# Performance work log

Measured on AMD Instinct MI355X. Metric: run time of the kernel, lower is better.

## Reference

```python
import jax, jax.numpy as jnp
import numpy as np


def setup_inputs() -> dict:
    key = jax.random.key(0)
    k1, k2 = jax.random.split(key)
    C, K, H, W = 512, 150, 512, 512
    feats_chw = jax.random.normal(k1, (C, H, W), dtype=jnp.float32)
    class_logits_chw = jax.random.normal(k2, (K, H, W), dtype=jnp.float32)
    return {"feats_chw": feats_chw, "class_logits_chw": class_logits_chw}


def reference(feats_chw, class_logits_chw):
    Cf, H, W = feats_chw.shape
    K = class_logits_chw.shape[0]
    N = H * W
    feats = feats_chw.reshape(Cf, N).T                      # (N, C)
    logits = class_logits_chw.reshape(K, N).T               # (N, K)
    probs = jax.nn.softmax(logits, axis=-1)                 # softmax over classes per pixel
    # normalize each class column over all N pixels
    weights = probs / jnp.clip(jnp.sum(probs, axis=0, keepdims=True), 1e-06)
    context = jnp.einsum('nk,nc->kc', weights, feats)        # (K, C)
    return context
```

## Files before the change

kernel.cpp:

```cpp
#include <hip/hip_runtime.h>
#include <hip/hip_bf16.h>


#define N_PIX (512 * 512)
#define K_CLS 150
#define C_DIM 512
#define NBLK 256
#define PIX_PER_BLK (N_PIX / NBLK)
#define CHUNK 64
#define NCHUNK (PIX_PER_BLK / CHUNK)

typedef short short8 __attribute__((ext_vector_type(8)));
typedef float floatx4 __attribute__((ext_vector_type(4)));

__device__ __forceinline__ unsigned short f2bf(float x) {
  unsigned u = __builtin_bit_cast(unsigned, x);
  u += 0x7FFFu + ((u >> 16) & 1u);
  return (unsigned short)(u >> 16);
}

__device__ __forceinline__ void async_ld4(const float* g, float* l) {
  __builtin_amdgcn_global_load_lds(
      (const __attribute__((address_space(1))) void*)g,
      (__attribute__((address_space(3))) void*)l, 4, 0, 0);
}

__global__ __launch_bounds__(512) void sg_main(
    const float* __restrict__ feats, const float* __restrict__ logits,
    float* __restrict__ ctx, float* __restrict__ colsum_g)
{
  __shared__ float lraw[2][K_CLS][CHUNK];
  __shared__ unsigned short atile[20 * 64 * 8];
  __shared__ float part[8][64];
  __shared__ float colsum_lds[K_CLS];

  const int tid  = threadIdx.x;
  const int w    = tid >> 6;
  const int lane = tid & 63;
  const int quad = lane >> 4;
  const int l15  = lane & 15;
  const int nbase = blockIdx.x * PIX_PER_BLK;

  for (int i = tid; i < 20 * 64 * 8 / 2; i += 512) ((unsigned*)atile)[i] = 0u;
  if (tid < K_CLS) colsum_lds[tid] = 0.f;

  floatx4 acc[4][10];
#pragma unroll
  for (int j = 0; j < 4; ++j)
#pragma unroll
    for (int rg = 0; rg < 10; ++rg)
      acc[j][rg] = (floatx4){0.f, 0.f, 0.f, 0.f};

#pragma unroll
  for (int i = 0; i < 19; ++i) {
    const int k = w + 8 * i;
    if (k < K_CLS)
      async_ld4(logits + (size_t)k * N_PIX + nbase + lane, &lraw[0][k][0]);
  }

  for (int ci = 0; ci < NCHUNK; ++ci) {
    __syncthreads();
    const int buf = ci & 1;
    const int n0  = nbase + ci * CHUNK;

    floatx4 breg[8];
#pragma unroll
    for (int j = 0; j < 4; ++j) {
      const float* bp = feats + (size_t)((w + 8 * j) * 16 + l15) * N_PIX + n0 + quad * 8;
      breg[2 * j]     = *(const floatx4*)bp;
      breg[2 * j + 1] = *(const floatx4*)(bp + 4);
    }

    float s_part = 0.f;
#pragma unroll
    for (int i = 0; i < 19; ++i) {
      const int k = w + 8 * i;
      if (k < K_CLS) s_part += __expf(lraw[buf][k][lane]);
    }
    part[w][lane] = s_part;
    __syncthreads();
    float s = 0.f;
#pragma unroll
    for (int ww = 0; ww < 8; ++ww) s += part[ww][lane];
    const float rs = 1.0f / s;

#pragma unroll
    for (int i = 0; i < 19; ++i) {
      const int k = w + 8 * i;
      if (k < K_CLS) {
        const float p = __expf(lraw[buf][k][lane]) * rs;
        const int fid = ((k >> 4) << 1) + (lane >> 5);
        const int lin = (k & 15) | (((lane >> 3) & 3) << 4);
        atile[(fid * 64 + lin) * 8 + (lane & 7)] = f2bf(p);
        float r = p;
        r += __shfl_xor(r, 32);
        r += __shfl_xor(r, 16);
        r += __shfl_xor(r, 8);
        r += __shfl_xor(r, 4);
        r += __shfl_xor(r, 2);
        r += __shfl_xor(r, 1);
        if (lane == 0) colsum_lds[k] += r;
      }
    }
    __syncthreads();

    short8 bfrag[4];
#pragma unroll
    for (int j = 0; j < 4; ++j) {
      floatx4 lo = breg[2 * j], hi = breg[2 * j + 1];
      short8 f;
      f[0] = f2bf(lo[0]); f[1] = f2bf(lo[1]); f[2] = f2bf(lo[2]); f[3] = f2bf(lo[3]);
      f[4] = f2bf(hi[0]); f[5] = f2bf(hi[1]); f[6] = f2bf(hi[2]); f[7] = f2bf(hi[3]);
      bfrag[j] = f;
    }

#pragma unroll
    for (int j = 0; j < 4; ++j) {
      const float* bp = feats + (size_t)((w + 8 * j) * 16 + l15) * N_PIX + n0 + 32 + quad * 8;
      breg[2 * j]     = *(const floatx4*)bp;
      breg[2 * j + 1] = *(const floatx4*)(bp + 4);
    }

    if (ci + 1 < NCHUNK) {
#pragma unroll
      for (int i = 0; i < 19; ++i) {
        const int k = w + 8 * i;
        if (k < K_CLS)
          async_ld4(logits + (size_t)k * N_PIX + n0 + CHUNK + lane, &lraw[buf ^ 1][k][0]);
      }
    }

#pragma unroll
    for (int rg = 0; rg < 10; ++rg) {
      short8 afrag = *(const short8*)&atile[((rg * 2 + 0) * 64 + lane) * 8];
#pragma unroll
      for (int j = 0; j < 4; ++j)
        acc[j][rg] = __builtin_amdgcn_mfma_f32_16x16x32_bf16(afrag, bfrag[j], acc[j][rg], 0, 0, 0);
    }

#pragma unroll
    for (int j = 0; j < 4; ++j) {
      floatx4 lo = breg[2 * j], hi = breg[2 * j + 1];
      short8 f;
      f[0] = f2bf(lo[0]); f[1] = f2bf(lo[1]); f[2] = f2bf(lo[2]); f[3] = f2bf(lo[3]);
      f[4] = f2bf(hi[0]); f[5] = f2bf(hi[1]); f[6] = f2bf(hi[2]); f[7] = f2bf(hi[3]);
      bfrag[j] = f;
    }

#pragma unroll
    for (int rg = 0; rg < 10; ++rg) {
      short8 afrag = *(const short8*)&atile[((rg * 2 + 1) * 64 + lane) * 8];
#pragma unroll
      for (int j = 0; j < 4; ++j)
        acc[j][rg] = __builtin_amdgcn_mfma_f32_16x16x32_bf16(afrag, bfrag[j], acc[j][rg], 0, 0, 0);
    }
  }

#pragma unroll
  for (int j = 0; j < 4; ++j) {
    const int c = ((w + 8 * j) << 4) + l15;
#pragma unroll
    for (int rg = 0; rg < 10; ++rg) {
#pragma unroll
      for (int r = 0; r < 4; ++r) {
        const int row = rg * 16 + quad * 4 + r;
        if (row < K_CLS) atomicAdd(&ctx[row * C_DIM + c], acc[j][rg][r]);
      }
    }
  }
  __syncthreads();
  if (tid < K_CLS) atomicAdd(&colsum_g[tid], colsum_lds[tid]);
}

__global__ void sg_epi(const float* __restrict__ ctx, const float* __restrict__ colsum,
                       float* __restrict__ out)
{
  const int idx = blockIdx.x * 256 + threadIdx.x;
  if (idx < K_CLS * C_DIM) {
    const float d = fmaxf(colsum[idx >> 9], 1e-6f);
    out[idx] = ctx[idx] / d;
  }
}

extern "C" void kernel_launch(void* const* d_in, const int* in_sizes, int n_in,
                              void* d_out, int out_size, void* d_ws, size_t ws_size,
                              hipStream_t stream)
{
  const float* feats  = (const float*)d_in[0];
  const float* logits = (const float*)d_in[1];
  float* ctx    = (float*)d_ws;
  float* colsum = ctx + K_CLS * C_DIM;
  hipMemsetAsync(d_ws, 0, (K_CLS * C_DIM + K_CLS) * sizeof(float), stream);
  sg_main<<<dim3(NBLK), dim3(512), 0, stream>>>(feats, logits, ctx, colsum);
  sg_epi<<<dim3((K_CLS * C_DIM + 255) / 256), dim3(256), 0, stream>>>(ctx, colsum, (float*)d_out);
}
```

Before: 938.4 us.

## Split softmax and GEMM into separate kernels with bf16 probability buffer

Adds a two-kernel path: a softmax kernel computes per-pixel class probabilities, writes them as bf16 to a workspace buffer and accumulates column sums. A separate GEMM kernel then streams feats and the bf16 probabilities over more blocks, splitting channels across block pairs. This aims to raise parallelism and occupancy over the single fused kernel limited to 256 blocks. In exchange it adds extra global memory traffic for the intermediate buffer and needs a large workspace, falling back to the old kernel otherwise.

Result: no change. 930.1 us (-0.9%).

```diff
diff --git a/kernel.cpp b/kernel.cpp
--- a/kernel.cpp
+++ b/kernel.cpp
@@ -5,25 +5,227 @@
 #define N_PIX (512 * 512)
 #define K_CLS 150
 #define C_DIM 512
+#define KPAD 160
+
+typedef short short8 __attribute__((ext_vector_type(8)));
+typedef float floatx4 __attribute__((ext_vector_type(4)));
+
+__device__ __forceinline__ unsigned short f2bf(float x) {
+  unsigned u = __builtin_bit_cast(unsigned, x);
+  u += 0x7FFFu + ((u >> 16) & 1u);
+  return (unsigned short)(u >> 16);
+}
+
+__device__ __forceinline__ void async_ld16(const void* g, void* l) {
+  __builtin_amdgcn_global_load_lds(
+      (const __attribute__((address_space(1))) void*)g,
+      (__attribute__((address_space(3))) void*)l, 16, 0, 0);
+}
+__device__ __forceinline__ void async_ld4(const void* g, void* l) {
+  __builtin_amdgcn_global_load_lds(
+      (const __attribute__((address_space(1))) void*)g,
+      (__attribute__((address_space(3))) void*)l, 4, 0, 0);
+}
+
+#define K1_PIX 256
+#define K1_NCH 8
+
+__global__ __launch_bounds__(512, 6) void sg_softmax(
+    const float* __restrict__ logits, unsigned short* __restrict__ pg,
+    float* __restrict__ colsum_g)
+{
+  __shared__ float lraw[2][152][32];
+  __shared__ float part[16][32];
+  __shared__ float csum[K_CLS];
+
+  const int tid  = threadIdx.x;
+  const int w    = tid >> 6;
+  const int lane = tid & 63;
+  const int hi   = lane >> 5;
+  const int px   = lane & 31;
+  const int nbase = blockIdx.x * K1_PIX;
+
+  if (tid < K_CLS) csum[tid] = 0.f;
+
+  auto stage = [&](int ci, int buf) {
+#pragma unroll
+    for (int u = 0; u < 3; ++u) {
+      const int t = w + 8 * u;
+      if (t < 19) {
+        int row = 8 * t + (lane >> 3);
+        if (row > 149) row = 149;
+        async_ld16(logits + (size_t)row * N_PIX + nbase + ci * 32 + (lane & 7) * 4,
+                   &lraw[buf][8 * t][0]);
+      }
+    }
+  };
+  stage(0, 0);
+
+  for (int ci = 0; ci < K1_NCH; ++ci) {
+    const int buf = ci & 1;
+    __syncthreads();
+
+    float sp = 0.f;
+    const int g = 2 * w + hi;
+#pragma unroll
+    for (int i = 0; i < 10; ++i) {
+      const int k = g + 16 * i;
+      if (k < K_CLS) sp += __expf(lraw[buf][k][px]);
+    }
+    part[g][px] = sp;
+    __syncthreads();
+    float s = 0.f;
+#pragma unroll
+    for (int gg = 0; gg < 16; ++gg) s += part[gg][px];
+    const float rs = 1.0f / s;
+
+    if (ci + 1 < K1_NCH) stage(ci + 1, buf ^ 1);
+
+#pragma unroll
+    for (int i = 0; i < 10; ++i) {
+      const int k = w + 16 * i + 8 * hi;
+      if (k < K_CLS) {
+        const float p = __expf(lraw[buf][k][px]) * rs;
+        pg[(size_t)k * N_PIX + nbase + ci * 32 + px] = f2bf(p);
+        float r = p;
+        r += __shfl_xor(r, 16);
+        r += __shfl_xor(r, 8);
+        r += __shfl_xor(r, 4);
+        r += __shfl_xor(r, 2);
+        r += __shfl_xor(r, 1);
+        if (px == 0) csum[k] += r;
+      }
+    }
+  }
+  __syncthreads();
+  if (tid < K_CLS) atomicAdd(&colsum_g[tid], csum[tid]);
+}
+
+#define K2_PIX 1024
+#define K2_NCH 16
+
+__global__ __launch_bounds__(512, 4) void sg_gemm(
+    const float* __restrict__ feats, const unsigned short* __restrict__ pg,
+    float* __restrict__ ctx)
+{
+  __shared__ unsigned short atile[2][20 * 64 * 8];
+
+  const int tid  = threadIdx.x;
+  const int w    = tid >> 6;
+  const int lane = tid & 63;
+  const int quad = lane >> 4;
+  const int l15  = lane & 15;
+  const int pxbase = (blockIdx.x >> 1) * K2_PIX;
+  const int cbase  = (blockIdx.x & 1) * 256;
+
+  auto stage = [&](int ci, int buf) {
+#pragma unroll
+    for (int u = 0; u < 3; ++u) {
+      const int t = w + 8 * u;
+      if (t < 20) {
+        const int rg = t >> 1, ks = t & 1;
+        async_ld16(pg + (size_t)(rg * 16 + l15) * N_PIX + pxbase + ci * 64 + ks * 32 + quad * 8,
+                   &atile[buf][t * 512]);
+      }
+    }
+  };
+
+  floatx4 acc[2][10];
+#pragma unroll
+  for (int j = 0; j < 2; ++j)
+#pragma unroll
+    for (int rg = 0; rg < 10; ++rg)
+      acc[j][rg] = (floatx4){0.f, 0.f, 0.f, 0.f};
+
+  stage(0, 0);
+
+  for (int ci = 0; ci < K2_NCH; ++ci) {
+    const int buf = ci & 1;
+    const int n0  = pxbase + ci * 64;
+    __syncthreads();
+
+    floatx4 breg[4];
+#pragma unroll
+    for (int j = 0; j < 2; ++j) {
+      const float* bp = feats + (size_t)(cbase + (w + 8 * j) * 16 + l15) * N_PIX + n0 + quad * 8;
+      breg[2 * j]     = *(const floatx4*)bp;
+      breg[2 * j + 1] = *(const floatx4*)(bp + 4);
+    }
+
+    if (ci + 1 < K2_NCH) stage(ci + 1, buf ^ 1);
+
+    short8 bfrag[2];
+#pragma unroll
+    for (int j = 0; j < 2; ++j) {
+      floatx4 lo = breg[2 * j], hi = breg[2 * j + 1];
+      short8 f;
+      f[0] = f2bf(lo[0]); f[1] = f2bf(lo[1]); f[2] = f2bf(lo[2]); f[3] = f2bf(lo[3]);
+      f[4] = f2bf(hi[0]); f[5] = f2bf(hi[1]); f[6] = f2bf(hi[2]); f[7] = f2bf(hi[3]);
+      bfrag[j] = f;
+    }
+
+    floatx4 breg2[4];
+#pragma unroll
+    for (int j = 0; j < 2; ++j) {
+      const float* bp = feats + (size_t)(cbase + (w + 8 * j) * 16 + l15) * N_PIX + n0 + 32 + quad * 8;
+      breg2[2 * j]     = *(const floatx4*)bp;
+      breg2[2 * j + 1] = *(const floatx4*)(bp + 4);
+    }
+
+#pragma unroll
+    for (int rg = 0; rg < 10; ++rg) {
+      short8 afrag = *(const short8*)&atile[buf][(rg * 2 + 0) * 512 + lane * 8];
+#pragma unroll
+      for (int j = 0; j < 2; ++j)
+        acc[j][rg] = __builtin_amdgcn_mfma_f32_16x16x32_bf16(afrag, bfrag[j], acc[j][rg], 0, 0, 0);
+    }
+
+#pragma unroll
+    for (int j = 0; j < 2; ++j) {
+      floatx4 lo = breg2[2 * j], hi = breg2[2 * j + 1];
+      short8 f;
+      f[0] = f2bf(lo[0]); f[1] = f2bf(lo[1]); f[2] = f2bf(lo[2]); f[3] = f2bf(lo[3]);
+      f[4] = f2bf(hi[0]); f[5] = f2bf(hi[1]); f[6] = f2bf(hi[2]); f[7] = f2bf(hi[3]);
+      bfrag[j] = f;
+    }
+
+#pragma unroll
+    for (int rg = 0; rg < 10; ++rg) {
+      short8 afrag = *(const short8*)&atile[buf][(rg * 2 + 1) * 512 + lane * 8];
+#pragma unroll
+      for (int j = 0; j < 2; ++j)
+        acc[j][rg] = __builtin_amdgcn_mfma_f32_16x16x32_bf16(afrag, bfrag[j], acc[j][rg], 0, 0, 0);
+    }
+  }
+
+#pragma unroll
+  for (int j = 0; j < 2; ++j) {
+    const int c = cbase + ((w + 8 * j) << 4) + l15;
+#pragma unroll
+    for (int rg = 0; rg < 10; ++rg) {
+#pragma unroll
+      for (int r = 0; r < 4; ++r) {
+        const int row = rg * 16 + quad * 4 + r;
+        if (row < K_CLS) atomicAdd(&ctx[row * C_DIM + c], acc[j][rg][r]);
+      }
+    }
+  }
+}
+
+__global__ void sg_epi(const float* __restrict__ ctx, const float* __restrict__ colsum,
+                       float* __restrict__ out)
+{
+  const int idx = blockIdx.x * 256 + threadIdx.x;
+  if (idx < K_CLS * C_DIM) {
+    const float d = fmaxf(colsum[idx >> 9], 1e-6f);
+    out[idx] = ctx[idx] / d;
+  }
+}
+
 #define NBLK 256
 #define PIX_PER_BLK (N_PIX / NBLK)
 #define CHUNK 64
 #define NCHUNK (PIX_PER_BLK / CHUNK)
-
-typedef short short8 __attribute__((ext_vector_type(8)));
-typedef float floatx4 __attribute__((ext_vector_type(4)));
-
-__device__ __forceinline__ unsigned short f2bf(float x) {
-  unsigned u = __builtin_bit_cast(unsigned, x);
-  u += 0x7FFFu + ((u >> 16) & 1u);
-  return (unsigned short)(u >> 16);
-}
-
-__device__ __forceinline__ void async_ld4(const float* g, float* l) {
-  __builtin_amdgcn_global_load_lds(
-      (const __attribute__((address_space(1))) void*)g,
-      (__attribute__((address_space(3))) void*)l, 4, 0, 0);
-}
 
 __global__ __launch_bounds__(512) void sg_main(
     const float* __restrict__ feats, const float* __restrict__ logits,
@@ -172,25 +374,29 @@
   if (tid < K_CLS) atomicAdd(&colsum_g[tid], colsum_lds[tid]);
 }
 
-__global__ void sg_epi(const float* __restrict__ ctx, const float* __restrict__ colsum,
-                       float* __restrict__ out)
-{
-  const int idx = blockIdx.x * 256 + threadIdx.x;
-  if (idx < K_CLS * C_DIM) {
-    const float d = fmaxf(colsum[idx >> 9], 1e-6f);
-    out[idx] = ctx[idx] / d;
-  }
-}
-
 extern "C" void kernel_launch(void* const* d_in, const int* in_sizes, int n_in,
                               void* d_out, int out_size, void* d_ws, size_t ws_size,
                               hipStream_t stream)
 {
   const float* feats  = (const float*)d_in[0];
   const float* logits = (const float*)d_in[1];
-  float* ctx    = (float*)d_ws;
-  float* colsum = ctx + K_CLS * C_DIM;
-  hipMemsetAsync(d_ws, 0, (K_CLS * C_DIM + K_CLS) * sizeof(float), stream);
-  sg_main<<<dim3(NBLK), dim3(512), 0, stream>>>(feats, logits, ctx, colsum);
-  sg_epi<<<dim3((K_CLS * C_DIM + 255) / 256), dim3(256), 0, stream>>>(ctx, colsum, (float*)d_out);
-}
+
+  const size_t pg_bytes = (size_t)KPAD * N_PIX * sizeof(unsigned short);
+  const size_t acc_bytes = (size_t)(K_CLS * C_DIM + K_CLS) * sizeof(float);
+
+  if (ws_size >= pg_bytes + acc_bytes) {
+    unsigned short* pg = (unsigned short*)d_ws;
+    float* ctx    = (float*)((char*)d_ws + pg_bytes);
+    float* colsum = ctx + K_CLS * C_DIM;
+    hipMemsetAsync(ctx, 0, acc_bytes, stream);
+    sg_softmax<<<dim3(1024), dim3(512), 0, stream>>>(logits, pg, colsum);
+    sg_gemm<<<dim3(512), dim3(512), 0, stream>>>(feats, pg, ctx);
+    sg_epi<<<dim3((K_CLS * C_DIM + 255) / 256), dim3(256), 0, stream>>>(ctx, colsum, (float*)d_out);
+  } else {
+    float* ctx    = (float*)d_ws;
+    float* colsum = ctx + K_CLS * C_DIM;
+    hipMemsetAsync(d_ws, 0, acc_bytes, stream);
+    sg_main<<<dim3(NBLK), dim3(512), 0, stream>>>(feats, logits, ctx, colsum);
+    sg_epi<<<dim3((K_CLS * C_DIM + 255) / 256), dim3(256), 0, stream>>>(ctx, colsum, (float*)d_out);
+  }
+}
```
